# Optimization experiments

Hardware: AMD Instinct MI355X
Metric: run time of the kernel (lower is better)

## Reference

```python
import jax, jax.numpy as jnp
import numpy as np

DIM = 64
HEADS = 8
DIM_HEAD = 64
INNER = HEADS * DIM_HEAD  # 512
FB, HB, WB = 3, 4, 4
Q_L = HB * WB            # 16
KV_L = FB * HB * WB      # 48
EPS = 1e-5


def conv3(x, W):
    # x: [N,Cin,H,W], W: [Cout,Cin,3,3], stride 1, pad 1, no bias
    return jax.lax.conv_general_dilated(
        x, W, window_strides=(1, 1), padding='SAME',
        dimension_numbers=('NCHW', 'OIHW', 'NCHW'))


def layernorm(x, g, b):
    # normalize over last (channel) dim, matching nn.LayerNorm(dim)
    mu = jnp.mean(x, axis=-1, keepdims=True)
    var = jnp.mean(jnp.square(x - mu), axis=-1, keepdims=True)
    return (x - mu) * jax.lax.rsqrt(var + EPS) * g + b


def warp_nearest(x, flow):
    # Faithful to flow_warp-style grid_sample(mode='nearest', padding='zeros',
    # align_corners=True): sample x at round(grid + flow), zeros out-of-range.
    n, c, h, w = x.shape
    gy, gx = jnp.meshgrid(jnp.arange(h, dtype=x.dtype),
                          jnp.arange(w, dtype=x.dtype), indexing='ij')
    px = gx[None] + flow[:, 0]  # [n,h,w]
    py = gy[None] + flow[:, 1]
    ix = jnp.round(px).astype(jnp.int32)
    iy = jnp.round(py).astype(jnp.int32)
    valid = (ix >= 0) & (ix < w) & (iy >= 0) & (iy < h)
    flat = jnp.clip(iy, 0, h - 1) * w + jnp.clip(ix, 0, w - 1)  # [n,h,w]

    def gather_one(xi, fi):
        return jnp.take(xi.reshape(c, h * w), fi.reshape(-1), axis=1).reshape(c, h, w)

    out = jax.vmap(gather_one)(x, flat)
    return out * valid[:, None].astype(x.dtype)


def setup_inputs() -> dict:
    key = jax.random.key(0)
    ks = jax.random.split(key, 12)
    b, h, w = 2, 128, 128
    inp = {
        'q_inp': jax.random.normal(ks[0], (b, 1, DIM, h, w), jnp.float32),
        'k_inp': jax.random.normal(ks[1], (b, 3, DIM, h, w), jnp.float32),
        'flow_f': jax.random.normal(ks[2], (b, 2, h, w), jnp.float32) * 4.0,
        'flow_b': jax.random.normal(ks[3], (b, 2, h, w), jnp.float32) * 4.0,
        'gq': jnp.ones((DIM,), jnp.float32),
        'bq': jnp.zeros((DIM,), jnp.float32),
        'gkv': jnp.ones((DIM,), jnp.float32),
        'bkv': jnp.zeros((DIM,), jnp.float32),
        'Wq': jax.random.normal(ks[4], (INNER, DIM, 3, 3), jnp.float32) * 0.02,
        'Wkv': jax.random.normal(ks[5], (2 * INNER, DIM, 3, 3), jnp.float32) * 0.02,
        'Wout': jax.random.normal(ks[6], (DIM, INNER, 3, 3), jnp.float32) * 0.02,
        'static_a': jax.random.truncated_normal(ks[7], -2.0, 2.0, (1, HEADS, Q_L, KV_L), jnp.float32),
    }
    return inp


def _fgsw_msa(q_inp, k_inp, flow_f, flow_b, gq, bq, gkv, bkv, Wq, Wkv, Wout, static_a):
    b, f_q, c, h, w = q_inp.shape
    # flow-guided warp of forward/backward key frames (nearest, zeros padding)
    k_f = warp_nearest(k_inp[:, 0], flow_f)
    k_r = k_inp[:, 1]
    k_b = warp_nearest(k_inp[:, 2], flow_b)
    k_stack = jnp.stack([k_f, k_r, k_b], axis=1)  # [b,3,c,h,w]

    # LayerNorm over channels
    qn = layernorm(q_inp.transpose(0, 1, 3, 4, 2), gq, bq).transpose(0, 1, 4, 2, 3)
    kvn = layernorm(k_stack.transpose(0, 1, 3, 4, 2), gkv, bkv).transpose(0, 1, 4, 2, 3)

    # conv QKV projections
    q = conv3(qn.reshape(b * f_q, c, h, w), Wq)       # [b, INNER, h, w]
    kv = conv3(kvn.reshape(b * 3, c, h, w), Wkv)      # [3b, 2*INNER, h, w]
    k, v = jnp.split(kv, 2, axis=1)

    nh, nw = h // HB, w // WB

    def part(t, f):
        # [(b f), C, H, W] -> [(b nh nw), heads, f*HB*WB, d]
        C = t.shape[1]
        t = t.reshape(b, f, C, nh, HB, nw, WB)
        t = t.transpose(0, 3, 5, 1, 4, 6, 2)  # b, nh, nw, f, p1, p2, C
        t = t.reshape(b * nh * nw, f * HB * WB, HEADS, C // HEADS)
        return t.transpose(0, 2, 1, 3)

    qh = part(q, f_q) * (DIM_HEAD ** -0.5)
    kh = part(k, 3)
    vh = part(v, 3)

    sim = jnp.einsum('bhid,bhjd->bhij', qh, kh) + static_a
    attn = jax.nn.softmax(sim, axis=-1)
    out = jnp.einsum('bhij,bhjd->bhid', attn, vh)  # [(b nh nw), heads, Q_L, d]

    out = out.transpose(0, 2, 1, 3).reshape(b * nh * nw, f_q * HB * WB, INNER)
    out = out.reshape(b, nh, nw, f_q, HB, WB, INNER)
    out = out.transpose(0, 3, 6, 1, 4, 2, 5).reshape(b * f_q, INNER, h, w)
    out = conv3(out, Wout).reshape(b, f_q, c, h, w)
    return out


def reference(q_inp, k_inp, flow_f, flow_b, gq, bq, gkv, bkv, Wq, Wkv, Wout, static_a):
    return _fgsw_msa(q_inp, k_inp, flow_f, flow_b, gq, bq, gkv, bkv, Wq, Wkv, Wout, static_a)
```

## Files before the change

### kernel.cpp

```cpp
#include <hip/hip_runtime.h>


typedef __attribute__((ext_vector_type(8))) short bf16x8;
typedef __attribute__((ext_vector_type(4))) float f32x4;

__device__ __forceinline__ float bs2f(unsigned short s) {
    return __uint_as_float(((unsigned int)s) << 16);
}
__device__ __forceinline__ unsigned short f2bs(float f) {
    unsigned int u = __float_as_uint(f);
    u += 0x7fffu + ((u >> 16) & 1u);
    return (unsigned short)(u >> 16);
}

__global__ __launch_bounds__(256) void ln_q_kernel(
    const float* __restrict__ q_inp, const float* __restrict__ g,
    const float* __restrict__ b, unsigned short* __restrict__ qn)
{
    int wid  = (blockIdx.x * 256 + threadIdx.x) >> 6;
    int lane = threadIdx.x & 63;
    int pix  = wid & 16383;
    int bb   = wid >> 14;
    float val = q_inp[(bb * 64 + lane) * 16384 + pix];
    float s = val;
    #pragma unroll
    for (int m = 1; m < 64; m <<= 1) s += __shfl_xor(s, m);
    float mu = s * (1.f / 64.f);
    float d = val - mu;
    float s2 = d * d;
    #pragma unroll
    for (int m = 1; m < 64; m <<= 1) s2 += __shfl_xor(s2, m);
    float o = d * rsqrtf(s2 * (1.f / 64.f) + 1e-5f) * g[lane] + b[lane];
    qn[wid * 64 + lane] = f2bs(o);
}

__global__ __launch_bounds__(256) void warp_ln_kv_kernel(
    const float* __restrict__ k_inp, const float* __restrict__ flow_f,
    const float* __restrict__ flow_b, const float* __restrict__ g,
    const float* __restrict__ b, unsigned short* __restrict__ kvn)
{
    int wid  = (blockIdx.x * 256 + threadIdx.x) >> 6;
    int lane = threadIdx.x & 63;
    int x  = wid & 127;
    int y  = (wid >> 7) & 127;
    int bf = wid >> 14;
    int f  = bf % 3, bb = bf / 3;
    float val;
    if (f == 1) {
        val = k_inp[(bf * 64 + lane) * 16384 + y * 128 + x];
    } else {
        const float* fl = (f == 0) ? flow_f : flow_b;
        float fx = fl[(bb * 2 + 0) * 16384 + y * 128 + x];
        float fy = fl[(bb * 2 + 1) * 16384 + y * 128 + x];
        int ix = (int)rintf((float)x + fx);
        int iy = (int)rintf((float)y + fy);
        if (ix >= 0 && ix < 128 && iy >= 0 && iy < 128)
            val = k_inp[(bf * 64 + lane) * 16384 + iy * 128 + ix];
        else
            val = 0.f;
    }
    float s = val;
    #pragma unroll
    for (int m = 1; m < 64; m <<= 1) s += __shfl_xor(s, m);
    float mu = s * (1.f / 64.f);
    float d = val - mu;
    float s2 = d * d;
    #pragma unroll
    for (int m = 1; m < 64; m <<= 1) s2 += __shfl_xor(s2, m);
    float o = d * rsqrtf(s2 * (1.f / 64.f) + 1e-5f) * g[lane] + b[lane];
    kvn[wid * 64 + lane] = f2bs(o);
}

__global__ __launch_bounds__(256) void repack_bf16_kernel(
    const float* __restrict__ w, unsigned short* __restrict__ wp,
    int IC, int total)
{
    int idx = blockIdx.x * 256 + threadIdx.x;
    if (idx >= total) return;
    int tap = idx % 9;
    int tmp = idx / 9;
    int ic  = tmp % IC;
    int oc  = tmp / IC;
    wp[oc * IC * 9 + (ic >> 6) * 576 + tap * 64 + (ic & 63)] = f2bs(w[idx]);
}

__global__ __launch_bounds__(512) void qconv_kernel(
    const unsigned short* __restrict__ qn,
    const unsigned short* __restrict__ wq,
    unsigned short* __restrict__ qc)
{
    __shared__ __align__(16) unsigned short patch[100 * 80];
    const int tid = threadIdx.x, lane = tid & 63, w = tid >> 6;
    const int tx = blockIdx.x & 15, ty = blockIdx.x >> 4;
    const int img = blockIdx.y;
    const int gx0 = tx * 8 - 1, gy0 = ty * 8 - 1;
    const int r = lane & 15, kg = lane >> 4;
    const int m = w >> 1, nh = w & 1;

    for (int u = tid; u < 800; u += 512) {
        int pos = u >> 3, seg = u & 7;
        int hy = pos / 10, hx = pos - hy * 10;
        int gy = gy0 + hy, gx = gx0 + hx;
        uint4 v = make_uint4(0u, 0u, 0u, 0u);
        if ((unsigned)gy < 128u && (unsigned)gx < 128u)
            v = *reinterpret_cast<const uint4*>(
                qn + ((img * 128 + gy) * 128 + gx) * 64 + seg * 8);
        *reinterpret_cast<uint4*>(patch + pos * 80 + seg * 8) = v;
    }
    __syncthreads();

    f32x4 acc[16];
    #pragma unroll
    for (int n = 0; n < 16; ++n) acc[n] = f32x4{0.f, 0.f, 0.f, 0.f};

    #pragma unroll 2
    for (int kk = 0; kk < 18; ++kk) {
        int tap = kk >> 1, ic0 = (kk & 1) * 32;
        int ky = tap / 3, kx = tap - ky * 3;
        int pos = (m * 2 + (r >> 3) + ky) * 10 + (r & 7) + kx;
        bf16x8 a = *reinterpret_cast<const bf16x8*>(patch + pos * 80 + ic0 + kg * 8);
        #pragma unroll
        for (int n = 0; n < 16; ++n) {
            bf16x8 b = *reinterpret_cast<const bf16x8*>(
                wq + (size_t)(nh * 256 + n * 16 + r) * 576 + kk * 32 + kg * 8);
            acc[n] = __builtin_amdgcn_mfma_f32_16x16x32_bf16(a, b, acc[n], 0, 0, 0);
        }
    }
    #pragma unroll
    for (int n = 0; n < 16; ++n) {
        #pragma unroll
        for (int reg = 0; reg < 4; ++reg) {
            int p = m * 16 + kg * 4 + reg;
            int y = ty * 8 + (p >> 3), x = tx * 8 + (p & 7);
            qc[((size_t)(img * 128 + y) * 128 + x) * 512 + nh * 256 + n * 16 + r] =
                f2bs(0.125f * acc[n][reg]);
        }
    }
}

__global__ __launch_bounds__(256, 4) void fused_attn_kernel(
    const unsigned short* __restrict__ kvn,
    const unsigned short* __restrict__ wkv,
    const float* __restrict__ sa,
    unsigned short* __restrict__ qcao)
{
    __shared__ __align__(16) unsigned char smem[35712];
    unsigned short* kvp   = (unsigned short*)smem;
    unsigned short* kls   = (unsigned short*)(smem + 17280);
    unsigned short* vls_T = (unsigned short*)(smem + 24192);
    unsigned short* pls   = (unsigned short*)(smem + 33408);

    const int tid  = threadIdx.x;
    const int lane = tid & 63;
    const int w    = tid >> 6;
    const int wx = blockIdx.x & 31, wy = blockIdx.x >> 5;
    const int bb = blockIdx.y;
    const int gx0 = wx * 4 - 1, gy0 = wy * 4 - 1;

    for (int u = tid; u < 864; u += 256) {
        int f = u / 288, rest = u - f * 288;
        int pos = rest >> 3, seg = rest & 7;
        int hy = pos / 6, hx = pos - hy * 6;
        int gy = gy0 + hy, gx = gx0 + hx;
        uint4 v = make_uint4(0u, 0u, 0u, 0u);
        if ((unsigned)gy < 128u && (unsigned)gx < 128u)
            v = *reinterpret_cast<const uint4*>(
                kvn + (((bb * 3 + f) * 128 + gy) * 128 + gx) * 64 + seg * 8);
        *reinterpret_cast<uint4*>(kvp + (f * 36 + pos) * 80 + seg * 8) = v;
    }
    for (int u = tid; u < 1024; u += 256) {
        int row = u >> 4, c = 48 + (u & 15);
        vls_T[row * 72 + c] = 0;
    }
    {
        int row = tid >> 4, c = 48 + (tid & 15);
        pls[row * 72 + c] = 0;
    }
    __syncthreads();

    const int r  = lane & 15;
    const int kg = lane >> 4;
    const int py = r >> 2, px = r & 3;
    const int is_v = w >> 1, pair = w & 1;

    const unsigned short* qbase =
        qcao + ((size_t)(bb * 128 + wy * 4 + (r >> 2)) * 128 + wx * 4 + (r & 3)) * 512;

    f32x4 oacc = {0.f, 0.f, 0.f, 0.f};

    for (int h = 0; h < 8; ++h) {
        if (h > 0) {
            #pragma unroll
            for (int reg = 0; reg < 4; ++reg) {
                int i = kg * 4 + reg;
                int y = wy * 4 + (i >> 2), x = wx * 4 + (i & 3);
                qcao[((size_t)(bb * 128 + y) * 128 + x) * 512 + (h - 1) * 64 + w * 16 + r] =
                    f2bs(oacc[reg]);
            }
        }

        {
            const int ocb = is_v * 512 + h * 64 + pair * 32;
            const unsigned short* wb = wkv + (size_t)ocb * 576 + kg * 8;
            bf16x8 nb0 = *reinterpret_cast<const bf16x8*>(wb + (size_t)r * 576);
            bf16x8 nb1 = *reinterpret_cast<const bf16x8*>(wb + (size_t)(16 + r) * 576);
            f32x4 c00 = {0.f,0.f,0.f,0.f}, c01 = c00, c10 = c00, c11 = c00, c20 = c00, c21 = c00;
            #pragma unroll 2
            for (int kk = 0; kk < 18; ++kk) {
                bf16x8 b0 = nb0, b1 = nb1;
                if (kk < 17) {
                    nb0 = *reinterpret_cast<const bf16x8*>(wb + (size_t)r * 576 + (kk + 1) * 32);
                    nb1 = *reinterpret_cast<const bf16x8*>(wb + (size_t)(16 + r) * 576 + (kk + 1) * 32);
                }
                int tap = kk >> 1, ic0 = (kk & 1) * 32;
                int ky = tap / 3, kx = tap - ky * 3;
                int pos = (py + ky) * 6 + (px + kx);
                bf16x8 a0 = *reinterpret_cast<const bf16x8*>(kvp + pos * 80 + ic0 + kg * 8);
                bf16x8 a1 = *reinterpret_cast<const bf16x8*>(kvp + (36 + pos) * 80 + ic0 + kg * 8);
                bf16x8 a2 = *reinterpret_cast<const bf16x8*>(kvp + (72 + pos) * 80 + ic0 + kg * 8);
                c00 = __builtin_amdgcn_mfma_f32_16x16x32_bf16(a0, b0, c00, 0, 0, 0);
                c10 = __builtin_amdgcn_mfma_f32_16x16x32_bf16(a1, b0, c10, 0, 0, 0);
                c20 = __builtin_amdgcn_mfma_f32_16x16x32_bf16(a2, b0, c20, 0, 0, 0);
                c01 = __builtin_amdgcn_mfma_f32_16x16x32_bf16(a0, b1, c01, 0, 0, 0);
                c11 = __builtin_amdgcn_mfma_f32_16x16x32_bf16(a1, b1, c11, 0, 0, 0);
                c21 = __builtin_amdgcn_mfma_f32_16x16x32_bf16(a2, b1, c21, 0, 0, 0);
            }
            if (!is_v) {
                #pragma unroll
                for (int reg = 0; reg < 4; ++reg) {
                    int jr = kg * 4 + reg;
                    int cb = pair * 32 + r;
                    kls[(jr +  0) * 72 + cb]      = f2bs(c00[reg]);
                    kls[(jr + 16) * 72 + cb]      = f2bs(c10[reg]);
                    kls[(jr + 32) * 72 + cb]      = f2bs(c20[reg]);
                    kls[(jr +  0) * 72 + cb + 16] = f2bs(c01[reg]);
                    kls[(jr + 16) * 72 + cb + 16] = f2bs(c11[reg]);
                    kls[(jr + 32) * 72 + cb + 16] = f2bs(c21[reg]);
                }
            } else {
                #pragma unroll
                for (int reg = 0; reg < 4; ++reg) {
                    int jr = kg * 4 + reg;
                    int d0 = pair * 32 + r;
                    vls_T[d0 * 72        + jr]      = f2bs(c00[reg]);
                    vls_T[d0 * 72        + 16 + jr] = f2bs(c10[reg]);
                    vls_T[d0 * 72        + 32 + jr] = f2bs(c20[reg]);
                    vls_T[(d0 + 16) * 72 + jr]      = f2bs(c01[reg]);
                    vls_T[(d0 + 16) * 72 + 16 + jr] = f2bs(c11[reg]);
                    vls_T[(d0 + 16) * 72 + 32 + jr] = f2bs(c21[reg]);
                }
            }
        }
        __syncthreads();

        {
            bf16x8 qa0 = *reinterpret_cast<const bf16x8*>(qbase + h * 64 + kg * 8);
            bf16x8 qa1 = *reinterpret_cast<const bf16x8*>(qbase + h * 64 + 32 + kg * 8);
            f32x4 s0 = {0.f,0.f,0.f,0.f}, s1 = s0, s2 = s0;
            #pragma unroll
            for (int t = 0; t < 3; ++t) {
                bf16x8 b0 = *reinterpret_cast<const bf16x8*>(kls + (t * 16 + r) * 72 + kg * 8);
                bf16x8 b1 = *reinterpret_cast<const bf16x8*>(kls + (t * 16 + r) * 72 + 32 + kg * 8);
                f32x4& st = (t == 0) ? s0 : (t == 1) ? s1 : s2;
                st = __builtin_amdgcn_mfma_f32_16x16x32_bf16(qa0, b0, st, 0, 0, 0);
                st = __builtin_amdgcn_mfma_f32_16x16x32_bf16(qa1, b1, st, 0, 0, 0);
            }
            #pragma unroll
            for (int reg = 0; reg < 4; ++reg) {
                int i = kg * 4 + reg;
                float v0 = s0[reg] + sa[(h * 16 + i) * 48 + r];
                float v1 = s1[reg] + sa[(h * 16 + i) * 48 + 16 + r];
                float v2 = s2[reg] + sa[(h * 16 + i) * 48 + 32 + r];
                float mx = fmaxf(v0, fmaxf(v1, v2));
                #pragma unroll
                for (int m = 1; m < 16; m <<= 1) mx = fmaxf(mx, __shfl_xor(mx, m));
                float e0 = __expf(v0 - mx), e1 = __expf(v1 - mx), e2 = __expf(v2 - mx);
                float sum = e0 + e1 + e2;
                #pragma unroll
                for (int m = 1; m < 16; m <<= 1) sum += __shfl_xor(sum, m);
                float inv = 1.f / sum;
                pls[i * 72 + r]      = f2bs(e0 * inv);
                pls[i * 72 + 16 + r] = f2bs(e1 * inv);
                pls[i * 72 + 32 + r] = f2bs(e2 * inv);
            }
        }

        {
            bf16x8 pa0 = *reinterpret_cast<const bf16x8*>(pls + r * 72 + kg * 8);
            bf16x8 pa1 = *reinterpret_cast<const bf16x8*>(pls + r * 72 + 32 + kg * 8);
            bf16x8 vb0 = *reinterpret_cast<const bf16x8*>(vls_T + (w * 16 + r) * 72 + kg * 8);
            bf16x8 vb1 = *reinterpret_cast<const bf16x8*>(vls_T + (w * 16 + r) * 72 + 32 + kg * 8);
            f32x4 o = {0.f, 0.f, 0.f, 0.f};
            o = __builtin_amdgcn_mfma_f32_16x16x32_bf16(pa0, vb0, o, 0, 0, 0);
            o = __builtin_amdgcn_mfma_f32_16x16x32_bf16(pa1, vb1, o, 0, 0, 0);
            oacc = o;
        }
        __syncthreads();
    }
    #pragma unroll
    for (int reg = 0; reg < 4; ++reg) {
        int i = kg * 4 + reg;
        int y = wy * 4 + (i >> 2), x = wx * 4 + (i & 3);
        qcao[((size_t)(bb * 128 + y) * 128 + x) * 512 + 7 * 64 + w * 16 + r] = f2bs(oacc[reg]);
    }
}

__global__ __launch_bounds__(256) void conv512_kernel(
    const unsigned short* __restrict__ in,
    const unsigned short* __restrict__ wp,
    float* __restrict__ out)
{
    __shared__ __align__(16) unsigned short patch[100 * 80];
    const int tid = threadIdx.x, lane = tid & 63, w = tid >> 6;
    const int tx = blockIdx.x & 15, ty = blockIdx.x >> 4;
    const int img = blockIdx.y;
    const int gx0 = tx * 8 - 1, gy0 = ty * 8 - 1;
    const int r = lane & 15, kg = lane >> 4;

    f32x4 acc0 = {0.f,0.f,0.f,0.f}, acc1 = acc0, acc2 = acc0, acc3 = acc0;

    for (int ci = 0; ci < 8; ++ci) {
        __syncthreads();
        for (int u = tid; u < 800; u += 256) {
            int pos = u >> 3, seg = u & 7;
            int hy = pos / 10, hx = pos - hy * 10;
            int gy = gy0 + hy, gx = gx0 + hx;
            uint4 v = make_uint4(0u, 0u, 0u, 0u);
            if ((unsigned)gy < 128u && (unsigned)gx < 128u)
                v = *reinterpret_cast<const uint4*>(
                    in + (((size_t)img * 128 + gy) * 128 + gx) * 512 + ci * 64 + seg * 8);
            *reinterpret_cast<uint4*>(patch + pos * 80 + seg * 8) = v;
        }
        __syncthreads();
        #pragma unroll 3
        for (int kk = 0; kk < 18; ++kk) {
            int tap = kk >> 1, ic0 = (kk & 1) * 32;
            int ky = tap / 3, kx = tap - ky * 3;
            int oc = w * 16 + r;
            bf16x8 b = *reinterpret_cast<const bf16x8*>(
                wp + (size_t)oc * 4608 + ci * 576 + kk * 32 + kg * 8);
            #pragma unroll
            for (int m = 0; m < 4; ++m) {
                int rr = m * 16 + r;
                int pos = ((rr >> 3) + ky) * 10 + (rr & 7) + kx;
                bf16x8 a = *reinterpret_cast<const bf16x8*>(patch + pos * 80 + ic0 + kg * 8);
                f32x4& acc = (m == 0) ? acc0 : (m == 1) ? acc1 : (m == 2) ? acc2 : acc3;
                acc = __builtin_amdgcn_mfma_f32_16x16x32_bf16(a, b, acc, 0, 0, 0);
            }
        }
    }
    const int oc = w * 16 + r;
    #pragma unroll
    for (int m = 0; m < 4; ++m) {
        const f32x4& acc = (m == 0) ? acc0 : (m == 1) ? acc1 : (m == 2) ? acc2 : acc3;
        int r0 = m * 16 + kg * 4;
        int gy = ty * 8 + (r0 >> 3), gx = tx * 8 + (r0 & 7);
        *reinterpret_cast<float4*>(
            out + (((size_t)img * 64 + oc) * 128 + gy) * 128 + gx) =
            make_float4(acc[0], acc[1], acc[2], acc[3]);
    }
}

extern "C" void kernel_launch(void* const* d_in, const int* in_sizes, int n_in,
                              void* d_out, int out_size, void* d_ws, size_t ws_size,
                              hipStream_t stream)
{
    const float* q_inp  = (const float*)d_in[0];
    const float* k_inp  = (const float*)d_in[1];
    const float* flow_f = (const float*)d_in[2];
    const float* flow_b = (const float*)d_in[3];
    const float* gq     = (const float*)d_in[4];
    const float* bq     = (const float*)d_in[5];
    const float* gkv    = (const float*)d_in[6];
    const float* bkv    = (const float*)d_in[7];
    const float* Wq     = (const float*)d_in[8];
    const float* Wkv    = (const float*)d_in[9];
    const float* Wout   = (const float*)d_in[10];
    const float* sa     = (const float*)d_in[11];

    if (ws_size < 55050240u) return;

    char* ws = (char*)d_ws;
    unsigned short* qn   = (unsigned short*)(ws + 0);
    unsigned short* kvn  = (unsigned short*)(ws + 4194304);
    unsigned short* qcao = (unsigned short*)(ws + 16777216);
    unsigned short* wqb  = (unsigned short*)(ws + 50331648);
    unsigned short* wkvb = (unsigned short*)(ws + 50921472);
    unsigned short* wopb = (unsigned short*)(ws + 52101120);

    ln_q_kernel<<<8192, 256, 0, stream>>>(q_inp, gq, bq, qn);
    warp_ln_kv_kernel<<<24576, 256, 0, stream>>>(k_inp, flow_f, flow_b, gkv, bkv, kvn);

    repack_bf16_kernel<<<1152, 256, 0, stream>>>(Wq,   wqb,  64,  294912);
    repack_bf16_kernel<<<2304, 256, 0, stream>>>(Wkv,  wkvb, 64,  589824);
    repack_bf16_kernel<<<1152, 256, 0, stream>>>(Wout, wopb, 512, 294912);

    qconv_kernel<<<dim3(256, 2), 512, 0, stream>>>(qn, wqb, qcao);

    fused_attn_kernel<<<dim3(1024, 2), 256, 0, stream>>>(kvn, wkvb, sa, qcao);

    conv512_kernel<<<dim3(256, 2), 256, 0, stream>>>(qcao, wopb, (float*)d_out);
}
```

Baseline: 622.3 us.

## Merge prep kernels, pad LDS rows, prefetch Q and bias, restructure MFMA loops

Merges the two layernorm kernels into one launch and the three weight-repack kernels into one, cutting launch count. Widens the LDS row stride from 80 to 88 shorts in all conv/attention patch buffers so the strided ds_read_b128 accesses hit fewer bank conflicts. The attention kernel now prefetches the next head's Q fragments and loads the static bias into registers ahead of use. The conv inner loops are unrolled over pairs of 32-channel halves with double-buffered weight loads. Together these add register pressure and slightly more shared memory in exchange for fewer launches and better latency hiding.

```diff
diff --git a/kernel.cpp b/kernel.cpp
--- a/kernel.cpp
+++ b/kernel.cpp
@@ -13,15 +13,42 @@
     return (unsigned short)(u >> 16);
 }
 
-__global__ __launch_bounds__(256) void ln_q_kernel(
-    const float* __restrict__ q_inp, const float* __restrict__ g,
-    const float* __restrict__ b, unsigned short* __restrict__ qn)
+__global__ __launch_bounds__(256) void ln_all_kernel(
+    const float* __restrict__ q_inp, const float* __restrict__ k_inp,
+    const float* __restrict__ flow_f, const float* __restrict__ flow_b,
+    const float* __restrict__ gq, const float* __restrict__ bq,
+    const float* __restrict__ gkv, const float* __restrict__ bkv,
+    unsigned short* __restrict__ qn, unsigned short* __restrict__ kvn)
 {
     int wid  = (blockIdx.x * 256 + threadIdx.x) >> 6;
     int lane = threadIdx.x & 63;
-    int pix  = wid & 16383;
-    int bb   = wid >> 14;
-    float val = q_inp[(bb * 64 + lane) * 16384 + pix];
+    float val, gg, bbv;
+    unsigned short* dst;
+    if (wid < 32768) {
+        int pix = wid & 16383, bb = wid >> 14;
+        val = q_inp[(bb * 64 + lane) * 16384 + pix];
+        gg = gq[lane]; bbv = bq[lane];
+        dst = qn + wid * 64 + lane;
+    } else {
+        int kw = wid - 32768;
+        int x = kw & 127, y = (kw >> 7) & 127, bf = kw >> 14;
+        int f = bf % 3, bb = bf / 3;
+        if (f == 1) {
+            val = k_inp[(bf * 64 + lane) * 16384 + y * 128 + x];
+        } else {
+            const float* fl = (f == 0) ? flow_f : flow_b;
+            float fx = fl[(bb * 2 + 0) * 16384 + y * 128 + x];
+            float fy = fl[(bb * 2 + 1) * 16384 + y * 128 + x];
+            int ix = (int)rintf((float)x + fx);
+            int iy = (int)rintf((float)y + fy);
+            if (ix >= 0 && ix < 128 && iy >= 0 && iy < 128)
+                val = k_inp[(bf * 64 + lane) * 16384 + iy * 128 + ix];
+            else
+                val = 0.f;
+        }
+        gg = gkv[lane]; bbv = bkv[lane];
+        dst = kvn + kw * 64 + lane;
+    }
     float s = val;
     #pragma unroll
     for (int m = 1; m < 64; m <<= 1) s += __shfl_xor(s, m);
@@ -30,66 +57,36 @@
     float s2 = d * d;
     #pragma unroll
     for (int m = 1; m < 64; m <<= 1) s2 += __shfl_xor(s2, m);
-    float o = d * rsqrtf(s2 * (1.f / 64.f) + 1e-5f) * g[lane] + b[lane];
-    qn[wid * 64 + lane] = f2bs(o);
-}
-
-__global__ __launch_bounds__(256) void warp_ln_kv_kernel(
-    const float* __restrict__ k_inp, const float* __restrict__ flow_f,
-    const float* __restrict__ flow_b, const float* __restrict__ g,
-    const float* __restrict__ b, unsigned short* __restrict__ kvn)
-{
-    int wid  = (blockIdx.x * 256 + threadIdx.x) >> 6;
-    int lane = threadIdx.x & 63;
-    int x  = wid & 127;
-    int y  = (wid >> 7) & 127;
-    int bf = wid >> 14;
-    int f  = bf % 3, bb = bf / 3;
-    float val;
-    if (f == 1) {
-        val = k_inp[(bf * 64 + lane) * 16384 + y * 128 + x];
-    } else {
-        const float* fl = (f == 0) ? flow_f : flow_b;
-        float fx = fl[(bb * 2 + 0) * 16384 + y * 128 + x];
-        float fy = fl[(bb * 2 + 1) * 16384 + y * 128 + x];
-        int ix = (int)rintf((float)x + fx);
-        int iy = (int)rintf((float)y + fy);
-        if (ix >= 0 && ix < 128 && iy >= 0 && iy < 128)
-            val = k_inp[(bf * 64 + lane) * 16384 + iy * 128 + ix];
-        else
-            val = 0.f;
-    }
-    float s = val;
-    #pragma unroll
-    for (int m = 1; m < 64; m <<= 1) s += __shfl_xor(s, m);
-    float mu = s * (1.f / 64.f);
-    float d = val - mu;
-    float s2 = d * d;
-    #pragma unroll
-    for (int m = 1; m < 64; m <<= 1) s2 += __shfl_xor(s2, m);
-    float o = d * rsqrtf(s2 * (1.f / 64.f) + 1e-5f) * g[lane] + b[lane];
-    kvn[wid * 64 + lane] = f2bs(o);
-}
-
-__global__ __launch_bounds__(256) void repack_bf16_kernel(
-    const float* __restrict__ w, unsigned short* __restrict__ wp,
-    int IC, int total)
-{
-    int idx = blockIdx.x * 256 + threadIdx.x;
-    if (idx >= total) return;
+    *dst = f2bs(d * rsqrtf(s2 * (1.f / 64.f) + 1e-5f) * gg + bbv);
+}
+
+__device__ __forceinline__ void repack_one(
+    const float* __restrict__ w, unsigned short* __restrict__ wp, int IC, int idx)
+{
     int tap = idx % 9;
     int tmp = idx / 9;
     int ic  = tmp % IC;
     int oc  = tmp / IC;
     wp[oc * IC * 9 + (ic >> 6) * 576 + tap * 64 + (ic & 63)] = f2bs(w[idx]);
 }
+__global__ __launch_bounds__(256) void repack_all_kernel(
+    const float* __restrict__ Wq, const float* __restrict__ Wkv,
+    const float* __restrict__ Wout,
+    unsigned short* __restrict__ wqb, unsigned short* __restrict__ wkvb,
+    unsigned short* __restrict__ wopb)
+{
+    int idx = blockIdx.x * 256 + threadIdx.x;
+    if (idx < 294912)        repack_one(Wq,   wqb,  64,  idx);
+    else if (idx < 884736)   repack_one(Wkv,  wkvb, 64,  idx - 294912);
+    else if (idx < 1179648)  repack_one(Wout, wopb, 512, idx - 884736);
+}
 
 __global__ __launch_bounds__(512) void qconv_kernel(
     const unsigned short* __restrict__ qn,
     const unsigned short* __restrict__ wq,
     unsigned short* __restrict__ qc)
 {
-    __shared__ __align__(16) unsigned short patch[100 * 80];
+    __shared__ __align__(16) unsigned short patch[100 * 88];
     const int tid = threadIdx.x, lane = tid & 63, w = tid >> 6;
     const int tx = blockIdx.x & 15, ty = blockIdx.x >> 4;
     const int img = blockIdx.y;
@@ -105,7 +102,7 @@
         if ((unsigned)gy < 128u && (unsigned)gx < 128u)
             v = *reinterpret_cast<const uint4*>(
                 qn + ((img * 128 + gy) * 128 + gx) * 64 + seg * 8);
-        *reinterpret_cast<uint4*>(patch + pos * 80 + seg * 8) = v;
+        *reinterpret_cast<uint4*>(patch + pos * 88 + seg * 8) = v;
     }
     __syncthreads();
 
@@ -118,7 +115,7 @@
         int tap = kk >> 1, ic0 = (kk & 1) * 32;
         int ky = tap / 3, kx = tap - ky * 3;
         int pos = (m * 2 + (r >> 3) + ky) * 10 + (r & 7) + kx;
-        bf16x8 a = *reinterpret_cast<const bf16x8*>(patch + pos * 80 + ic0 + kg * 8);
+        bf16x8 a = *reinterpret_cast<const bf16x8*>(patch + pos * 88 + ic0 + kg * 8);
         #pragma unroll
         for (int n = 0; n < 16; ++n) {
             bf16x8 b = *reinterpret_cast<const bf16x8*>(
@@ -144,11 +141,11 @@
     const float* __restrict__ sa,
     unsigned short* __restrict__ qcao)
 {
-    __shared__ __align__(16) unsigned char smem[35712];
+    __shared__ __align__(16) unsigned char smem[37440];
     unsigned short* kvp   = (unsigned short*)smem;
-    unsigned short* kls   = (unsigned short*)(smem + 17280);
-    unsigned short* vls_T = (unsigned short*)(smem + 24192);
-    unsigned short* pls   = (unsigned short*)(smem + 33408);
+    unsigned short* kls   = (unsigned short*)(smem + 19008);
+    unsigned short* vls_T = (unsigned short*)(smem + 25920);
+    unsigned short* pls   = (unsigned short*)(smem + 35136);
 
     const int tid  = threadIdx.x;
     const int lane = tid & 63;
@@ -166,7 +163,7 @@
         if ((unsigned)gy < 128u && (unsigned)gx < 128u)
             v = *reinterpret_cast<const uint4*>(
                 kvn + (((bb * 3 + f) * 128 + gy) * 128 + gx) * 64 + seg * 8);
-        *reinterpret_cast<uint4*>(kvp + (f * 36 + pos) * 80 + seg * 8) = v;
+        *reinterpret_cast<uint4*>(kvp + (f * 36 + pos) * 88 + seg * 8) = v;
     }
     for (int u = tid; u < 1024; u += 256) {
         int row = u >> 4, c = 48 + (u & 15);
@@ -186,9 +183,20 @@
     const unsigned short* qbase =
         qcao + ((size_t)(bb * 128 + wy * 4 + (r >> 2)) * 128 + wx * 4 + (r & 3)) * 512;
 
+    bf16x8 qa0c = *reinterpret_cast<const bf16x8*>(qbase + kg * 8);
+    bf16x8 qa1c = *reinterpret_cast<const bf16x8*>(qbase + 32 + kg * 8);
+    bf16x8 qa0n = qa0c, qa1n = qa1c;
+
     f32x4 oacc = {0.f, 0.f, 0.f, 0.f};
 
     for (int h = 0; h < 8; ++h) {
+        float sav[4][3];
+        #pragma unroll
+        for (int reg = 0; reg < 4; ++reg)
+            #pragma unroll
+            for (int t = 0; t < 3; ++t)
+                sav[reg][t] = sa[(h * 16 + kg * 4 + reg) * 48 + t * 16 + r];
+
         if (h > 0) {
             #pragma unroll
             for (int reg = 0; reg < 4; ++reg) {
@@ -199,31 +207,60 @@
             }
         }
 
+        if (h < 7) {
+            qa0n = *reinterpret_cast<const bf16x8*>(qbase + (h + 1) * 64 + kg * 8);
+            qa1n = *reinterpret_cast<const bf16x8*>(qbase + (h + 1) * 64 + 32 + kg * 8);
+        }
+
         {
             const int ocb = is_v * 512 + h * 64 + pair * 32;
-            const unsigned short* wb = wkv + (size_t)ocb * 576 + kg * 8;
-            bf16x8 nb0 = *reinterpret_cast<const bf16x8*>(wb + (size_t)r * 576);
-            bf16x8 nb1 = *reinterpret_cast<const bf16x8*>(wb + (size_t)(16 + r) * 576);
+            const unsigned short* wbr0 = wkv + (size_t)ocb * 576 + kg * 8 + (size_t)r * 576;
+            const unsigned short* wbr1 = wbr0 + (size_t)16 * 576;
+            bf16x8 bA0 = *reinterpret_cast<const bf16x8*>(wbr0);
+            bf16x8 bA1 = *reinterpret_cast<const bf16x8*>(wbr1);
+            bf16x8 bB0 = *reinterpret_cast<const bf16x8*>(wbr0 + 32);
+            bf16x8 bB1 = *reinterpret_cast<const bf16x8*>(wbr1 + 32);
             f32x4 c00 = {0.f,0.f,0.f,0.f}, c01 = c00, c10 = c00, c11 = c00, c20 = c00, c21 = c00;
-            #pragma unroll 2
-            for (int kk = 0; kk < 18; ++kk) {
-                bf16x8 b0 = nb0, b1 = nb1;
-                if (kk < 17) {
-                    nb0 = *reinterpret_cast<const bf16x8*>(wb + (size_t)r * 576 + (kk + 1) * 32);
-                    nb1 = *reinterpret_cast<const bf16x8*>(wb + (size_t)(16 + r) * 576 + (kk + 1) * 32);
-                }
-                int tap = kk >> 1, ic0 = (kk & 1) * 32;
-                int ky = tap / 3, kx = tap - ky * 3;
-                int pos = (py + ky) * 6 + (px + kx);
-                bf16x8 a0 = *reinterpret_cast<const bf16x8*>(kvp + pos * 80 + ic0 + kg * 8);
-                bf16x8 a1 = *reinterpret_cast<const bf16x8*>(kvp + (36 + pos) * 80 + ic0 + kg * 8);
-                bf16x8 a2 = *reinterpret_cast<const bf16x8*>(kvp + (72 + pos) * 80 + ic0 + kg * 8);
-                c00 = __builtin_amdgcn_mfma_f32_16x16x32_bf16(a0, b0, c00, 0, 0, 0);
-                c10 = __builtin_amdgcn_mfma_f32_16x16x32_bf16(a1, b0, c10, 0, 0, 0);
-                c20 = __builtin_amdgcn_mfma_f32_16x16x32_bf16(a2, b0, c20, 0, 0, 0);
-                c01 = __builtin_amdgcn_mfma_f32_16x16x32_bf16(a0, b1, c01, 0, 0, 0);
-                c11 = __builtin_amdgcn_mfma_f32_16x16x32_bf16(a1, b1, c11, 0, 0, 0);
-                c21 = __builtin_amdgcn_mfma_f32_16x16x32_bf16(a2, b1, c21, 0, 0, 0);
+            #pragma unroll
+            for (int kk2 = 0; kk2 < 18; kk2 += 2) {
+                {
+                    bf16x8 b0 = bA0, b1 = bA1;
+                    if (kk2 + 2 < 18) {
+                        bA0 = *reinterpret_cast<const bf16x8*>(wbr0 + (kk2 + 2) * 32);
+                        bA1 = *reinterpret_cast<const bf16x8*>(wbr1 + (kk2 + 2) * 32);
+                    }
+                    int tap = kk2 >> 1;
+                    int ky = tap / 3, kx = tap - ky * 3;
+                    int pos = (py + ky) * 6 + (px + kx);
+                    bf16x8 a0 = *reinterpret_cast<const bf16x8*>(kvp + pos * 88 + kg * 8);
+                    bf16x8 a1 = *reinterpret_cast<const bf16x8*>(kvp + (36 + pos) * 88 + kg * 8);
+                    bf16x8 a2 = *reinterpret_cast<const bf16x8*>(kvp + (72 + pos) * 88 + kg * 8);
+                    c00 = __builtin_amdgcn_mfma_f32_16x16x32_bf16(a0, b0, c00, 0, 0, 0);
+                    c10 = __builtin_amdgcn_mfma_f32_16x16x32_bf16(a1, b0, c10, 0, 0, 0);
+                    c20 = __builtin_amdgcn_mfma_f32_16x16x32_bf16(a2, b0, c20, 0, 0, 0);
+                    c01 = __builtin_amdgcn_mfma_f32_16x16x32_bf16(a0, b1, c01, 0, 0, 0);
+                    c11 = __builtin_amdgcn_mfma_f32_16x16x32_bf16(a1, b1, c11, 0, 0, 0);
+                    c21 = __builtin_amdgcn_mfma_f32_16x16x32_bf16(a2, b1, c21, 0, 0, 0);
+                }
+                {
+                    bf16x8 b0 = bB0, b1 = bB1;
+                    if (kk2 + 3 < 18) {
+                        bB0 = *reinterpret_cast<const bf16x8*>(wbr0 + (kk2 + 3) * 32);
+                        bB1 = *reinterpret_cast<const bf16x8*>(wbr1 + (kk2 + 3) * 32);
+                    }
+                    int tap = kk2 >> 1;
+                    int ky = tap / 3, kx = tap - ky * 3;
+                    int pos = (py + ky) * 6 + (px + kx);
+                    bf16x8 a0 = *reinterpret_cast<const bf16x8*>(kvp + pos * 88 + 32 + kg * 8);
+                    bf16x8 a1 = *reinterpret_cast<const bf16x8*>(kvp + (36 + pos) * 88 + 32 + kg * 8);
+                    bf16x8 a2 = *reinterpret_cast<const bf16x8*>(kvp + (72 + pos) * 88 + 32 + kg * 8);
+                    c00 = __builtin_amdgcn_mfma_f32_16x16x32_bf16(a0, b0, c00, 0, 0, 0);
+                    c10 = __builtin_amdgcn_mfma_f32_16x16x32_bf16(a1, b0, c10, 0, 0, 0);
+                    c20 = __builtin_amdgcn_mfma_f32_16x16x32_bf16(a2, b0, c20, 0, 0, 0);
+                    c01 = __builtin_amdgcn_mfma_f32_16x16x32_bf16(a0, b1, c01, 0, 0, 0);
+                    c11 = __builtin_amdgcn_mfma_f32_16x16x32_bf16(a1, b1, c11, 0, 0, 0);
+                    c21 = __builtin_amdgcn_mfma_f32_16x16x32_bf16(a2, b1, c21, 0, 0, 0);
+                }
             }
             if (!is_v) {
                 #pragma unroll
@@ -254,23 +291,21 @@
         __syncthreads();
 
         {
-            bf16x8 qa0 = *reinterpret_cast<const bf16x8*>(qbase + h * 64 + kg * 8);
-            bf16x8 qa1 = *reinterpret_cast<const bf16x8*>(qbase + h * 64 + 32 + kg * 8);
             f32x4 s0 = {0.f,0.f,0.f,0.f}, s1 = s0, s2 = s0;
             #pragma unroll
             for (int t = 0; t < 3; ++t) {
                 bf16x8 b0 = *reinterpret_cast<const bf16x8*>(kls + (t * 16 + r) * 72 + kg * 8);
                 bf16x8 b1 = *reinterpret_cast<const bf16x8*>(kls + (t * 16 + r) * 72 + 32 + kg * 8);
                 f32x4& st = (t == 0) ? s0 : (t == 1) ? s1 : s2;
-                st = __builtin_amdgcn_mfma_f32_16x16x32_bf16(qa0, b0, st, 0, 0, 0);
-                st = __builtin_amdgcn_mfma_f32_16x16x32_bf16(qa1, b1, st, 0, 0, 0);
+                st = __builtin_amdgcn_mfma_f32_16x16x32_bf16(qa0c, b0, st, 0, 0, 0);
+                st = __builtin_amdgcn_mfma_f32_16x16x32_bf16(qa1c, b1, st, 0, 0, 0);
             }
             #pragma unroll
             for (int reg = 0; reg < 4; ++reg) {
                 int i = kg * 4 + reg;
-                float v0 = s0[reg] + sa[(h * 16 + i) * 48 + r];
-                float v1 = s1[reg] + sa[(h * 16 + i) * 48 + 16 + r];
-                float v2 = s2[reg] + sa[(h * 16 + i) * 48 + 32 + r];
+                float v0 = s0[reg] + sav[reg][0];
+                float v1 = s1[reg] + sav[reg][1];
+                float v2 = s2[reg] + sav[reg][2];
                 float mx = fmaxf(v0, fmaxf(v1, v2));
                 #pragma unroll
                 for (int m = 1; m < 16; m <<= 1) mx = fmaxf(mx, __shfl_xor(mx, m));
@@ -295,6 +330,7 @@
             o = __builtin_amdgcn_mfma_f32_16x16x32_bf16(pa1, vb1, o, 0, 0, 0);
             oacc = o;
         }
+        qa0c = qa0n; qa1c = qa1n;
         __syncthreads();
     }
     #pragma unroll
@@ -310,14 +346,15 @@
     const unsigned short* __restrict__ wp,
     float* __restrict__ out)
 {
-    __shared__ __align__(16) unsigned short patch[100 * 80];
+    __shared__ __align__(16) unsigned short patch[100 * 88];
     const int tid = threadIdx.x, lane = tid & 63, w = tid >> 6;
     const int tx = blockIdx.x & 15, ty = blockIdx.x >> 4;
     const int img = blockIdx.y;
     const int gx0 = tx * 8 - 1, gy0 = ty * 8 - 1;
-    const int r = lane & 15, kg = lane >> 4;
+    const int r = lane & 15, kg = lane >> 6 == 0 ? lane >> 4 : lane >> 4;
 
     f32x4 acc0 = {0.f,0.f,0.f,0.f}, acc1 = acc0, acc2 = acc0, acc3 = acc0;
+    const int oc = w * 16 + r;
 
     for (int ci = 0; ci < 8; ++ci) {
         __syncthreads();
@@ -329,27 +366,44 @@
             if ((unsigned)gy < 128u && (unsigned)gx < 128u)
                 v = *reinterpret_cast<const uint4*>(
                     in + (((size_t)img * 128 + gy) * 128 + gx) * 512 + ci * 64 + seg * 8);
-            *reinterpret_cast<uint4*>(patch + pos * 80 + seg * 8) = v;
+            *reinterpret_cast<uint4*>(patch + pos * 88 + seg * 8) = v;
         }
         __syncthreads();
-        #pragma unroll 3
-        for (int kk = 0; kk < 18; ++kk) {
-            int tap = kk >> 1, ic0 = (kk & 1) * 32;
-            int ky = tap / 3, kx = tap - ky * 3;
-            int oc = w * 16 + r;
-            bf16x8 b = *reinterpret_cast<const bf16x8*>(
-                wp + (size_t)oc * 4608 + ci * 576 + kk * 32 + kg * 8);
-            #pragma unroll
-            for (int m = 0; m < 4; ++m) {
-                int rr = m * 16 + r;
-                int pos = ((rr >> 3) + ky) * 10 + (rr & 7) + kx;
-                bf16x8 a = *reinterpret_cast<const bf16x8*>(patch + pos * 80 + ic0 + kg * 8);
-                f32x4& acc = (m == 0) ? acc0 : (m == 1) ? acc1 : (m == 2) ? acc2 : acc3;
-                acc = __builtin_amdgcn_mfma_f32_16x16x32_bf16(a, b, acc, 0, 0, 0);
-            }
-        }
-    }
-    const int oc = w * 16 + r;
+        const unsigned short* wb = wp + (size_t)oc * 4608 + ci * 576 + kg * 8;
+        bf16x8 bA = *reinterpret_cast<const bf16x8*>(wb);
+        bf16x8 bB = *reinterpret_cast<const bf16x8*>(wb + 32);
+        #pragma unroll
+        for (int kk2 = 0; kk2 < 18; kk2 += 2) {
+            {
+                bf16x8 b = bA;
+                if (kk2 + 2 < 18) bA = *reinterpret_cast<const bf16x8*>(wb + (kk2 + 2) * 32);
+                int tap = kk2 >> 1;
+                int ky = tap / 3, kx = tap - ky * 3;
+                #pragma unroll
+                for (int m = 0; m < 4; ++m) {
+                    int rr = m * 16 + r;
+                    int pos = ((rr >> 3) + ky) * 10 + (rr & 7) + kx;
+                    bf16x8 a = *reinterpret_cast<const bf16x8*>(patch + pos * 88 + kg * 8);
+                    f32x4& acc = (m == 0) ? acc0 : (m == 1) ? acc1 : (m == 2) ? acc2 : acc3;
+                    acc = __builtin_amdgcn_mfma_f32_16x16x32_bf16(a, b, acc, 0, 0, 0);
+                }
+            }
+            {
+                bf16x8 b = bB;
+                if (kk2 + 3 < 18) bB = *reinterpret_cast<const bf16x8*>(wb + (kk2 + 3) * 32);
+                int tap = kk2 >> 1;
+                int ky = tap / 3, kx = tap - ky * 3;
+                #pragma unroll
+                for (int m = 0; m < 4; ++m) {
+                    int rr = m * 16 + r;
+                    int pos = ((rr >> 3) + ky) * 10 + (rr & 7) + kx;
+                    bf16x8 a = *reinterpret_cast<const bf16x8*>(patch + pos * 88 + 32 + kg * 8);
+                    f32x4& acc = (m == 0) ? acc0 : (m == 1) ? acc1 : (m == 2) ? acc2 : acc3;
+                    acc = __builtin_amdgcn_mfma_f32_16x16x32_bf16(a, b, acc, 0, 0, 0);
+                }
+            }
+        }
+    }
     #pragma unroll
     for (int m = 0; m < 4; ++m) {
         const f32x4& acc = (m == 0) ? acc0 : (m == 1) ? acc1 : (m == 2) ? acc2 : acc3;
@@ -388,12 +442,10 @@
     unsigned short* wkvb = (unsigned short*)(ws + 50921472);
     unsigned short* wopb = (unsigned short*)(ws + 52101120);
 
-    ln_q_kernel<<<8192, 256, 0, stream>>>(q_inp, gq, bq, qn);
-    warp_ln_kv_kernel<<<24576, 256, 0, stream>>>(k_inp, flow_f, flow_b, gkv, bkv, kvn);
-
-    repack_bf16_kernel<<<1152, 256, 0, stream>>>(Wq,   wqb,  64,  294912);
-    repack_bf16_kernel<<<2304, 256, 0, stream>>>(Wkv,  wkvb, 64,  589824);
-    repack_bf16_kernel<<<1152, 256, 0, stream>>>(Wout, wopb, 512, 294912);
+    ln_all_kernel<<<32768, 256, 0, stream>>>(q_inp, k_inp, flow_f, flow_b,
+                                             gq, bq, gkv, bkv, qn, kvn);
+
+    repack_all_kernel<<<4608, 256, 0, stream>>>(Wq, Wkv, Wout, wqb, wkvb, wopb);
 
     qconv_kernel<<<dim3(256, 2), 512, 0, stream>>>(qn, wqb, qcao);
 
```

Measured after the change: 608.6 us. -2.2%, faster.
